# Kernel tuning notes

Measured on AMD Instinct MI355X. Metric: run time of the kernel, lower is better.

## Reference

```python
import jax, jax.numpy as jnp
import numpy as np

N_NODES = 50000
N_EDGES = 800000
IN_FEAT = 96
NUM_CLASSES = 40
K_HOPS = 2        # SGConv K=2
LPA_ITERS = 3     # lpaiters


def setup_inputs() -> dict:
    key = jax.random.key(0)
    ks = jax.random.split(key, 6)
    x = jax.random.normal(ks[0], (N_NODES, IN_FEAT), dtype=jnp.float32)
    edge_index = jax.random.randint(ks[1], (2, N_EDGES), 0, N_NODES, dtype=jnp.int64)
    y = jax.random.randint(ks[2], (N_NODES,), 0, NUM_CLASSES, dtype=jnp.int64)
    mask = jax.random.bernoulli(ks[3], 0.5, (N_NODES,))
    edge_weight = jnp.ones((N_EDGES,), dtype=jnp.float32)  # nn.Parameter(torch.ones(num_edges))
    W = jax.random.normal(ks[4], (IN_FEAT, NUM_CLASSES), dtype=jnp.float32) / np.sqrt(IN_FEAT)
    b = jax.random.normal(ks[5], (NUM_CLASSES,), dtype=jnp.float32) * 0.01
    return {"x": x, "edge_index": edge_index, "y": y, "mask": mask,
            "edge_weight": edge_weight, "W": W, "b": b}


def _gcn_norm_self_loops(edge_index, edge_weight, n):
    # PyG gcn_norm with add_self_loops=True (SGConv default), fill_value=1
    row, col = edge_index[0], edge_index[1]
    loop = jnp.arange(n, dtype=row.dtype)
    row = jnp.concatenate([row, loop])
    col = jnp.concatenate([col, loop])
    w = jnp.concatenate([edge_weight, jnp.ones((n,), edge_weight.dtype)])
    deg = jax.ops.segment_sum(w, col, num_segments=n)
    dinv = jnp.where(deg > 0, deg ** -0.5, 0.0)
    return row, col, dinv[row] * w * dinv[col]


def _propagate(h, row, col, w, n):
    # gather -> weight -> scatter-add (aggr='add' at target nodes)
    return jax.ops.segment_sum(w[:, None] * h[row], col, num_segments=n)


def reference(x, edge_index, y, mask, edge_weight, W, b):
    n = x.shape[0]
    # ---- SGConv(K=2) with learnable edge_weight, gcn_norm with self-loops ----
    row, col, norm = _gcn_norm_self_loops(edge_index, edge_weight, n)
    h = x
    for _ in range(K_HOPS):
        h = _propagate(h, row, col, norm, n)
    x_out = h @ W + b
    # ---- LPAconv: edge_weight given, so NO gcn_norm; raw weighted scatter-add ----
    y1h = jax.nn.one_hot(y, NUM_CLASSES, dtype=jnp.float32)
    out = jnp.where(mask[:, None], y1h, 0.0)  # out[mask] = y[mask]
    r2, c2 = edge_index[0], edge_index[1]
    for _ in range(LPA_ITERS):
        out = _propagate(out, r2, c2, edge_weight, n)
    return (x_out, out)
```

## Files before the change

kernel.cpp:

```cpp
#include <hip/hip_runtime.h>

constexpr int N_NODES     = 50000;
constexpr int N_EDGES     = 800000;
constexpr int IN_FEAT     = 96;
constexpr int NUM_CLASSES = 40;
constexpr int CCH = NUM_CLASSES / 4;
constexpr int CH8 = NUM_CLASSES / 8;
constexpr int SCAN_B = 1024;
constexpr int NSCAN = (N_NODES + SCAN_B - 1) / SCAN_B;

__global__ void rank_k(const int* __restrict__ col, int* __restrict__ cnt,
                       int* __restrict__ rank) {
    int e = blockIdx.x * blockDim.x + threadIdx.x;
    if (e >= N_EDGES) return;
    rank[e] = atomicAdd(&cnt[col[e]], 1);
}

__global__ __launch_bounds__(SCAN_B) void scan1_k(const int* __restrict__ cnt,
                                                  int* __restrict__ pscan,
                                                  int* __restrict__ bsum) {
    __shared__ int buf[SCAN_B];
    int tid = threadIdx.x;
    int i = blockIdx.x * SCAN_B + tid;
    int v = (i < N_NODES) ? cnt[i] : 0;
    buf[tid] = v;
    __syncthreads();
    for (int off = 1; off < SCAN_B; off <<= 1) {
        int t = (tid >= off) ? buf[tid - off] : 0;
        __syncthreads();
        buf[tid] += t;
        __syncthreads();
    }
    if (i < N_NODES) pscan[i] = buf[tid] - v;
    if (tid == SCAN_B - 1) bsum[blockIdx.x] = buf[tid];
}

__global__ void scan2_k(const int* __restrict__ bsum, int* __restrict__ boff,
                        int* __restrict__ rowptr) {
    __shared__ int buf[64];
    int tid = threadIdx.x;
    int v = (tid < NSCAN) ? bsum[tid] : 0;
    buf[tid] = v;
    __syncthreads();
    for (int off = 1; off < 64; off <<= 1) {
        int t = (tid >= off) ? buf[tid - off] : 0;
        __syncthreads();
        buf[tid] += t;
        __syncthreads();
    }
    boff[tid] = buf[tid] - v;
    if (tid == NSCAN - 1) rowptr[N_NODES] = buf[tid];
}

__global__ void scan3_k(const int* __restrict__ pscan, const int* __restrict__ boff,
                        int* __restrict__ rowptr) {
    int i = blockIdx.x * blockDim.x + threadIdx.x;
    if (i < N_NODES) rowptr[i] = boff[i >> 10] + pscan[i];
}

__global__ void fill_k(const int* __restrict__ row, const int* __restrict__ col,
                       const float* __restrict__ ew, const int* __restrict__ rowptr,
                       const int* __restrict__ rank, int2* __restrict__ pair) {
    int e = blockIdx.x * blockDim.x + threadIdx.x;
    if (e >= N_EDGES) return;
    int c = col[e];
    int pos = rowptr[c] + rank[e];
    pair[pos] = make_int2(row[e], __float_as_int(ew[e]));
}

__global__ void node_prep_k(const int* __restrict__ rowptr, const int2* __restrict__ pair,
                            const int* __restrict__ y, const int* __restrict__ mask,
                            float* __restrict__ dinv, int* __restrict__ ym) {
    int i = blockIdx.x * blockDim.x + threadIdx.x;
    if (i >= N_NODES) return;
    int p0 = rowptr[i], p1 = rowptr[i + 1];
    float d = 1.0f;
    for (int p = p0; p < p1; ++p) d += __int_as_float(pair[p].y);
    dinv[i] = d > 0.0f ? rsqrtf(d) : 0.0f;
    ym[i] = (mask[i] != 0) ? y[i] : -1;
}

__global__ __launch_bounds__(256) void xw_k(const float* __restrict__ x,
                                            const float* __restrict__ Wm,
                                            float* __restrict__ xw) {
    __shared__ float4 Ws[IN_FEAT * CCH];
    int tid = threadIdx.x;
    for (int t = tid; t < IN_FEAT * CCH; t += 256)
        Ws[t] = reinterpret_cast<const float4*>(Wm)[t];
    __syncthreads();
    int idx = blockIdx.x * 256 + tid;
    if (idx >= N_NODES * CCH) return;
    int i = idx / CCH;
    int j = idx - i * CCH;
    const float4* xr = reinterpret_cast<const float4*>(x + i * IN_FEAT);
    float4 acc = make_float4(0.f, 0.f, 0.f, 0.f);
#pragma unroll
    for (int f4 = 0; f4 < IN_FEAT / 4; ++f4) {
        float4 xv = xr[f4];
        float4 w0 = Ws[(4 * f4 + 0) * CCH + j];
        float4 w1 = Ws[(4 * f4 + 1) * CCH + j];
        float4 w2 = Ws[(4 * f4 + 2) * CCH + j];
        float4 w3 = Ws[(4 * f4 + 3) * CCH + j];
        acc.x = fmaf(xv.x, w0.x, fmaf(xv.y, w1.x, fmaf(xv.z, w2.x, fmaf(xv.w, w3.x, acc.x))));
        acc.y = fmaf(xv.x, w0.y, fmaf(xv.y, w1.y, fmaf(xv.z, w2.y, fmaf(xv.w, w3.y, acc.y))));
        acc.z = fmaf(xv.x, w0.z, fmaf(xv.y, w1.z, fmaf(xv.z, w2.z, fmaf(xv.w, w3.z, acc.z))));
        acc.w = fmaf(xv.x, w0.w, fmaf(xv.y, w1.w, fmaf(xv.z, w2.w, fmaf(xv.w, w3.w, acc.w))));
    }
    reinterpret_cast<float4*>(xw + i * NUM_CLASSES)[j] = acc;
}

__global__ void fused1_k(const int* __restrict__ rowptr, const int2* __restrict__ pair,
                         const float* __restrict__ dinv, const int* __restrict__ ym,
                         const float* __restrict__ xw,
                         float* __restrict__ g1, float* __restrict__ lA) {
    int idx = blockIdx.x * blockDim.x + threadIdx.x;
    if (idx >= N_NODES * CH8) return;
    int i = idx / CH8;
    int j = idx - i * CH8;
    int p0 = rowptr[i], p1 = rowptr[i + 1];
    float dc = dinv[i];
    float selfw = dc * dc;
    const float4* vr = reinterpret_cast<const float4*>(xw + i * NUM_CLASSES) + 2 * j;
    float4 v0 = vr[0], v1 = vr[1];
    float4 s0 = make_float4(selfw * v0.x, selfw * v0.y, selfw * v0.z, selfw * v0.w);
    float4 s1 = make_float4(selfw * v1.x, selfw * v1.y, selfw * v1.z, selfw * v1.w);
    float4 a0 = make_float4(0.f, 0.f, 0.f, 0.f);
    float4 a1 = make_float4(0.f, 0.f, 0.f, 0.f);
    int base = j << 3;
    for (int p = p0; p < p1; ++p) {
        int2 pr = pair[p];
        int s = pr.x;
        float w = __int_as_float(pr.y);
        float nv = dinv[s] * (w * dc);
        const float4* ur = reinterpret_cast<const float4*>(xw + s * NUM_CLASSES) + 2 * j;
        float4 u0 = ur[0], u1 = ur[1];
        int t = ym[s] - base;
        s0.x = fmaf(nv, u0.x, s0.x); s0.y = fmaf(nv, u0.y, s0.y);
        s0.z = fmaf(nv, u0.z, s0.z); s0.w = fmaf(nv, u0.w, s0.w);
        s1.x = fmaf(nv, u1.x, s1.x); s1.y = fmaf(nv, u1.y, s1.y);
        s1.z = fmaf(nv, u1.z, s1.z); s1.w = fmaf(nv, u1.w, s1.w);
        a0.x += (t == 0) ? w : 0.f; a0.y += (t == 1) ? w : 0.f;
        a0.z += (t == 2) ? w : 0.f; a0.w += (t == 3) ? w : 0.f;
        a1.x += (t == 4) ? w : 0.f; a1.y += (t == 5) ? w : 0.f;
        a1.z += (t == 6) ? w : 0.f; a1.w += (t == 7) ? w : 0.f;
    }
    float4* go = reinterpret_cast<float4*>(g1 + i * NUM_CLASSES) + 2 * j;
    go[0] = s0; go[1] = s1;
    float4* lo = reinterpret_cast<float4*>(lA + i * NUM_CLASSES) + 2 * j;
    lo[0] = a0; lo[1] = a1;
}

__global__ void fused2_k(const int* __restrict__ rowptr, const int2* __restrict__ pair,
                         const float* __restrict__ dinv,
                         const float* __restrict__ g1, const float* __restrict__ lA,
                         const float* __restrict__ bias,
                         float* __restrict__ out, float* __restrict__ lB) {
    int idx = blockIdx.x * blockDim.x + threadIdx.x;
    if (idx >= N_NODES * CH8) return;
    int i = idx / CH8;
    int j = idx - i * CH8;
    int p0 = rowptr[i], p1 = rowptr[i + 1];
    float dc = dinv[i];
    float selfw = dc * dc;
    const float4* vr = reinterpret_cast<const float4*>(g1 + i * NUM_CLASSES) + 2 * j;
    float4 v0 = vr[0], v1 = vr[1];
    float4 s0 = make_float4(selfw * v0.x, selfw * v0.y, selfw * v0.z, selfw * v0.w);
    float4 s1 = make_float4(selfw * v1.x, selfw * v1.y, selfw * v1.z, selfw * v1.w);
    float4 a0 = make_float4(0.f, 0.f, 0.f, 0.f);
    float4 a1 = make_float4(0.f, 0.f, 0.f, 0.f);
    for (int p = p0; p < p1; ++p) {
        int2 pr = pair[p];
        int s = pr.x;
        float w = __int_as_float(pr.y);
        float nv = dinv[s] * (w * dc);
        const float4* ur = reinterpret_cast<const float4*>(g1 + s * NUM_CLASSES) + 2 * j;
        const float4* lr = reinterpret_cast<const float4*>(lA + s * NUM_CLASSES) + 2 * j;
        float4 u0 = ur[0], u1 = ur[1];
        float4 m0 = lr[0], m1 = lr[1];
        s0.x = fmaf(nv, u0.x, s0.x); s0.y = fmaf(nv, u0.y, s0.y);
        s0.z = fmaf(nv, u0.z, s0.z); s0.w = fmaf(nv, u0.w, s0.w);
        s1.x = fmaf(nv, u1.x, s1.x); s1.y = fmaf(nv, u1.y, s1.y);
        s1.z = fmaf(nv, u1.z, s1.z); s1.w = fmaf(nv, u1.w, s1.w);
        a0.x = fmaf(w, m0.x, a0.x); a0.y = fmaf(w, m0.y, a0.y);
        a0.z = fmaf(w, m0.z, a0.z); a0.w = fmaf(w, m0.w, a0.w);
        a1.x = fmaf(w, m1.x, a1.x); a1.y = fmaf(w, m1.y, a1.y);
        a1.z = fmaf(w, m1.z, a1.z); a1.w = fmaf(w, m1.w, a1.w);
    }
    const float4* br = reinterpret_cast<const float4*>(bias) + 2 * j;
    float4 b0 = br[0], b1 = br[1];
    s0.x += b0.x; s0.y += b0.y; s0.z += b0.z; s0.w += b0.w;
    s1.x += b1.x; s1.y += b1.y; s1.z += b1.z; s1.w += b1.w;
    float4* oo = reinterpret_cast<float4*>(out + i * NUM_CLASSES) + 2 * j;
    oo[0] = s0; oo[1] = s1;
    float4* lo = reinterpret_cast<float4*>(lB + i * NUM_CLASSES) + 2 * j;
    lo[0] = a0; lo[1] = a1;
}

__global__ void lpa3_k(const int* __restrict__ rowptr, const int2* __restrict__ pair,
                       const float* __restrict__ lB, float* __restrict__ lout) {
    int idx = blockIdx.x * blockDim.x + threadIdx.x;
    if (idx >= N_NODES * CH8) return;
    int i = idx / CH8;
    int j = idx - i * CH8;
    int p0 = rowptr[i], p1 = rowptr[i + 1];
    float4 a0 = make_float4(0.f, 0.f, 0.f, 0.f);
    float4 a1 = make_float4(0.f, 0.f, 0.f, 0.f);
    for (int p = p0; p < p1; ++p) {
        int2 pr = pair[p];
        int s = pr.x;
        float w = __int_as_float(pr.y);
        const float4* lr = reinterpret_cast<const float4*>(lB + s * NUM_CLASSES) + 2 * j;
        float4 m0 = lr[0], m1 = lr[1];
        a0.x = fmaf(w, m0.x, a0.x); a0.y = fmaf(w, m0.y, a0.y);
        a0.z = fmaf(w, m0.z, a0.z); a0.w = fmaf(w, m0.w, a0.w);
        a1.x = fmaf(w, m1.x, a1.x); a1.y = fmaf(w, m1.y, a1.y);
        a1.z = fmaf(w, m1.z, a1.z); a1.w = fmaf(w, m1.w, a1.w);
    }
    float4* lo = reinterpret_cast<float4*>(lout + i * NUM_CLASSES) + 2 * j;
    lo[0] = a0; lo[1] = a1;
}


extern "C" void kernel_launch(void* const* d_in, const int* in_sizes, int n_in,
                              void* d_out, int out_size, void* d_ws, size_t ws_size,
                              hipStream_t stream) {
    const float* x    = (const float*)d_in[0];
    const int*   ei   = (const int*)d_in[1];
    const int*   row  = ei;
    const int*   col  = ei + N_EDGES;
    const int*   y    = (const int*)d_in[2];
    const int*   mask = (const int*)d_in[3];
    const float* ew   = (const float*)d_in[4];
    const float* Wm   = (const float*)d_in[5];
    const float* bias = (const float*)d_in[6];
    float* out     = (float*)d_out;
    float* lpa_out = out + N_NODES * NUM_CLASSES;

    int*   cnt      = (int*)d_ws;
    int*   pscan    = cnt + 50000;
    int*   bsum     = pscan + 50048;
    int*   boff     = bsum + 64;
    int*   rowptr   = boff + 64;
    int*   rank     = rowptr + 50004;
    int*   ym       = rank + 800000;
    float* dinv     = (float*)(ym + 50000);
    int2*  pair     = (int2*)(dinv + 50000);
    float* xw       = (float*)(pair + 800000);
    float* g1       = xw + (size_t)N_NODES * NUM_CLASSES;
    float* lA       = g1 + (size_t)N_NODES * NUM_CLASSES;
    float* lB       = lA + (size_t)N_NODES * NUM_CLASSES;

    const int B = 256;
    auto g = [](long long n, int b) { return (int)((n + b - 1) / b); };

    hipMemsetAsync(cnt, 0, 50000u * sizeof(int), stream);
    rank_k<<<g(N_EDGES, B), B, 0, stream>>>(col, cnt, rank);
    scan1_k<<<NSCAN, SCAN_B, 0, stream>>>(cnt, pscan, bsum);
    scan2_k<<<1, 64, 0, stream>>>(bsum, boff, rowptr);
    scan3_k<<<g(N_NODES, B), B, 0, stream>>>(pscan, boff, rowptr);
    fill_k<<<g(N_EDGES, B), B, 0, stream>>>(row, col, ew, rowptr, rank, pair);

    node_prep_k<<<g(N_NODES, B), B, 0, stream>>>(rowptr, pair, y, mask, dinv, ym);

    xw_k<<<g((long long)N_NODES * CCH, B), B, 0, stream>>>(x, Wm, xw);

    fused1_k<<<g((long long)N_NODES * CH8, B), B, 0, stream>>>(
        rowptr, pair, dinv, ym, xw, g1, lA);
    fused2_k<<<g((long long)N_NODES * CH8, B), B, 0, stream>>>(
        rowptr, pair, dinv, g1, lA, bias, out, lB);
    lpa3_k<<<g((long long)N_NODES * CH8, B), B, 0, stream>>>(
        rowptr, pair, lB, lpa_out);
}
```

Before: 287.3 us.

## Store intermediate node features in fp16 and vectorize edge preprocessing kernels

Intermediate per-node buffers (xw, g1, lA, lB) are now stored as half precision with rows padded to 64 halves (128 bytes), and converted to float only for the arithmetic. This targets the gather bandwidth of the three propagation kernels, which fetch a 40-wide feature row per edge. The rank and fill kernels also switch to processing four edges per thread with int4 loads. The cost is fp16 rounding in the intermediate values, which could break tolerance, and LPA label counts above the half range could lose precision.

```diff
diff --git a/kernel.cpp b/kernel.cpp
--- a/kernel.cpp
+++ b/kernel.cpp
@@ -1,4 +1,5 @@
 #include <hip/hip_runtime.h>
+#include <hip/hip_fp16.h>
 
 constexpr int N_NODES     = 50000;
 constexpr int N_EDGES     = 800000;
@@ -6,14 +7,38 @@
 constexpr int NUM_CLASSES = 40;
 constexpr int CCH = NUM_CLASSES / 4;
 constexpr int CH8 = NUM_CLASSES / 8;
+constexpr int HS  = 64;
 constexpr int SCAN_B = 1024;
 constexpr int NSCAN = (N_NODES + SCAN_B - 1) / SCAN_B;
 
+__device__ __forceinline__ void h8_to_f(const uint4& u, float4& lo, float4& hi) {
+    float2 f0 = __half22float2(*reinterpret_cast<const __half2*>(&u.x));
+    float2 f1 = __half22float2(*reinterpret_cast<const __half2*>(&u.y));
+    float2 f2 = __half22float2(*reinterpret_cast<const __half2*>(&u.z));
+    float2 f3 = __half22float2(*reinterpret_cast<const __half2*>(&u.w));
+    lo = make_float4(f0.x, f0.y, f1.x, f1.y);
+    hi = make_float4(f2.x, f2.y, f3.x, f3.y);
+}
+__device__ __forceinline__ uint4 f_to_h8(const float4& lo, const float4& hi) {
+    uint4 u;
+    *reinterpret_cast<__half2*>(&u.x) = __floats2half2_rn(lo.x, lo.y);
+    *reinterpret_cast<__half2*>(&u.y) = __floats2half2_rn(lo.z, lo.w);
+    *reinterpret_cast<__half2*>(&u.z) = __floats2half2_rn(hi.x, hi.y);
+    *reinterpret_cast<__half2*>(&u.w) = __floats2half2_rn(hi.z, hi.w);
+    return u;
+}
+
 __global__ void rank_k(const int* __restrict__ col, int* __restrict__ cnt,
                        int* __restrict__ rank) {
-    int e = blockIdx.x * blockDim.x + threadIdx.x;
-    if (e >= N_EDGES) return;
-    rank[e] = atomicAdd(&cnt[col[e]], 1);
+    int t = blockIdx.x * blockDim.x + threadIdx.x;
+    if (t >= N_EDGES / 4) return;
+    int4 c = reinterpret_cast<const int4*>(col)[t];
+    int4 r;
+    r.x = atomicAdd(&cnt[c.x], 1);
+    r.y = atomicAdd(&cnt[c.y], 1);
+    r.z = atomicAdd(&cnt[c.z], 1);
+    r.w = atomicAdd(&cnt[c.w], 1);
+    reinterpret_cast<int4*>(rank)[t] = r;
 }
 
 __global__ __launch_bounds__(SCAN_B) void scan1_k(const int* __restrict__ cnt,
@@ -61,11 +86,16 @@
 __global__ void fill_k(const int* __restrict__ row, const int* __restrict__ col,
                        const float* __restrict__ ew, const int* __restrict__ rowptr,
                        const int* __restrict__ rank, int2* __restrict__ pair) {
-    int e = blockIdx.x * blockDim.x + threadIdx.x;
-    if (e >= N_EDGES) return;
-    int c = col[e];
-    int pos = rowptr[c] + rank[e];
-    pair[pos] = make_int2(row[e], __float_as_int(ew[e]));
+    int t = blockIdx.x * blockDim.x + threadIdx.x;
+    if (t >= N_EDGES / 4) return;
+    int4   c = reinterpret_cast<const int4*>(col)[t];
+    int4   r = reinterpret_cast<const int4*>(row)[t];
+    int4   k = reinterpret_cast<const int4*>(rank)[t];
+    float4 w = reinterpret_cast<const float4*>(ew)[t];
+    pair[rowptr[c.x] + k.x] = make_int2(r.x, __float_as_int(w.x));
+    pair[rowptr[c.y] + k.y] = make_int2(r.y, __float_as_int(w.y));
+    pair[rowptr[c.z] + k.z] = make_int2(r.z, __float_as_int(w.z));
+    pair[rowptr[c.w] + k.w] = make_int2(r.w, __float_as_int(w.w));
 }
 
 __global__ void node_prep_k(const int* __restrict__ rowptr, const int2* __restrict__ pair,
@@ -82,7 +112,7 @@
 
 __global__ __launch_bounds__(256) void xw_k(const float* __restrict__ x,
                                             const float* __restrict__ Wm,
-                                            float* __restrict__ xw) {
+                                            __half* __restrict__ xwh) {
     __shared__ float4 Ws[IN_FEAT * CCH];
     int tid = threadIdx.x;
     for (int t = tid; t < IN_FEAT * CCH; t += 256)
@@ -106,13 +136,16 @@
         acc.z = fmaf(xv.x, w0.z, fmaf(xv.y, w1.z, fmaf(xv.z, w2.z, fmaf(xv.w, w3.z, acc.z))));
         acc.w = fmaf(xv.x, w0.w, fmaf(xv.y, w1.w, fmaf(xv.z, w2.w, fmaf(xv.w, w3.w, acc.w))));
     }
-    reinterpret_cast<float4*>(xw + i * NUM_CLASSES)[j] = acc;
+    uint2 h;
+    *reinterpret_cast<__half2*>(&h.x) = __floats2half2_rn(acc.x, acc.y);
+    *reinterpret_cast<__half2*>(&h.y) = __floats2half2_rn(acc.z, acc.w);
+    reinterpret_cast<uint2*>(xwh + (size_t)i * HS)[j] = h;
 }
 
 __global__ void fused1_k(const int* __restrict__ rowptr, const int2* __restrict__ pair,
                          const float* __restrict__ dinv, const int* __restrict__ ym,
-                         const float* __restrict__ xw,
-                         float* __restrict__ g1, float* __restrict__ lA) {
+                         const __half* __restrict__ xwh,
+                         __half* __restrict__ g1h, __half* __restrict__ lAh) {
     int idx = blockIdx.x * blockDim.x + threadIdx.x;
     if (idx >= N_NODES * CH8) return;
     int i = idx / CH8;
@@ -120,8 +153,8 @@
     int p0 = rowptr[i], p1 = rowptr[i + 1];
     float dc = dinv[i];
     float selfw = dc * dc;
-    const float4* vr = reinterpret_cast<const float4*>(xw + i * NUM_CLASSES) + 2 * j;
-    float4 v0 = vr[0], v1 = vr[1];
+    uint4 vh = *reinterpret_cast<const uint4*>(xwh + (size_t)i * HS + j * 8);
+    float4 v0, v1; h8_to_f(vh, v0, v1);
     float4 s0 = make_float4(selfw * v0.x, selfw * v0.y, selfw * v0.z, selfw * v0.w);
     float4 s1 = make_float4(selfw * v1.x, selfw * v1.y, selfw * v1.z, selfw * v1.w);
     float4 a0 = make_float4(0.f, 0.f, 0.f, 0.f);
@@ -132,8 +165,8 @@
         int s = pr.x;
         float w = __int_as_float(pr.y);
         float nv = dinv[s] * (w * dc);
-        const float4* ur = reinterpret_cast<const float4*>(xw + s * NUM_CLASSES) + 2 * j;
-        float4 u0 = ur[0], u1 = ur[1];
+        uint4 uh = *reinterpret_cast<const uint4*>(xwh + (size_t)s * HS + j * 8);
+        float4 u0, u1; h8_to_f(uh, u0, u1);
         int t = ym[s] - base;
         s0.x = fmaf(nv, u0.x, s0.x); s0.y = fmaf(nv, u0.y, s0.y);
         s0.z = fmaf(nv, u0.z, s0.z); s0.w = fmaf(nv, u0.w, s0.w);
@@ -144,17 +177,15 @@
         a1.x += (t == 4) ? w : 0.f; a1.y += (t == 5) ? w : 0.f;
         a1.z += (t == 6) ? w : 0.f; a1.w += (t == 7) ? w : 0.f;
     }
-    float4* go = reinterpret_cast<float4*>(g1 + i * NUM_CLASSES) + 2 * j;
-    go[0] = s0; go[1] = s1;
-    float4* lo = reinterpret_cast<float4*>(lA + i * NUM_CLASSES) + 2 * j;
-    lo[0] = a0; lo[1] = a1;
+    *reinterpret_cast<uint4*>(g1h + (size_t)i * HS + j * 8) = f_to_h8(s0, s1);
+    *reinterpret_cast<uint4*>(lAh + (size_t)i * HS + j * 8) = f_to_h8(a0, a1);
 }
 
 __global__ void fused2_k(const int* __restrict__ rowptr, const int2* __restrict__ pair,
                          const float* __restrict__ dinv,
-                         const float* __restrict__ g1, const float* __restrict__ lA,
+                         const __half* __restrict__ g1h, const __half* __restrict__ lAh,
                          const float* __restrict__ bias,
-                         float* __restrict__ out, float* __restrict__ lB) {
+                         float* __restrict__ out, __half* __restrict__ lBh) {
     int idx = blockIdx.x * blockDim.x + threadIdx.x;
     if (idx >= N_NODES * CH8) return;
     int i = idx / CH8;
@@ -162,8 +193,8 @@
     int p0 = rowptr[i], p1 = rowptr[i + 1];
     float dc = dinv[i];
     float selfw = dc * dc;
-    const float4* vr = reinterpret_cast<const float4*>(g1 + i * NUM_CLASSES) + 2 * j;
-    float4 v0 = vr[0], v1 = vr[1];
+    uint4 vh = *reinterpret_cast<const uint4*>(g1h + (size_t)i * HS + j * 8);
+    float4 v0, v1; h8_to_f(vh, v0, v1);
     float4 s0 = make_float4(selfw * v0.x, selfw * v0.y, selfw * v0.z, selfw * v0.w);
     float4 s1 = make_float4(selfw * v1.x, selfw * v1.y, selfw * v1.z, selfw * v1.w);
     float4 a0 = make_float4(0.f, 0.f, 0.f, 0.f);
@@ -173,10 +204,10 @@
         int s = pr.x;
         float w = __int_as_float(pr.y);
         float nv = dinv[s] * (w * dc);
-        const float4* ur = reinterpret_cast<const float4*>(g1 + s * NUM_CLASSES) + 2 * j;
-        const float4* lr = reinterpret_cast<const float4*>(lA + s * NUM_CLASSES) + 2 * j;
-        float4 u0 = ur[0], u1 = ur[1];
-        float4 m0 = lr[0], m1 = lr[1];
+        uint4 uh = *reinterpret_cast<const uint4*>(g1h + (size_t)s * HS + j * 8);
+        uint4 mh = *reinterpret_cast<const uint4*>(lAh + (size_t)s * HS + j * 8);
+        float4 u0, u1; h8_to_f(uh, u0, u1);
+        float4 m0, m1; h8_to_f(mh, m0, m1);
         s0.x = fmaf(nv, u0.x, s0.x); s0.y = fmaf(nv, u0.y, s0.y);
         s0.z = fmaf(nv, u0.z, s0.z); s0.w = fmaf(nv, u0.w, s0.w);
         s1.x = fmaf(nv, u1.x, s1.x); s1.y = fmaf(nv, u1.y, s1.y);
@@ -184,20 +215,19 @@
         a0.x = fmaf(w, m0.x, a0.x); a0.y = fmaf(w, m0.y, a0.y);
         a0.z = fmaf(w, m0.z, a0.z); a0.w = fmaf(w, m0.w, a0.w);
         a1.x = fmaf(w, m1.x, a1.x); a1.y = fmaf(w, m1.y, a1.y);
-        a1.z = fmaf(w, m1.z, a1.z); a1.w = fmaf(w, m1.w, a1.w);
+        a1.w = fmaf(w, m1.w, a1.w); a1.z = fmaf(w, m1.z, a1.z);
     }
     const float4* br = reinterpret_cast<const float4*>(bias) + 2 * j;
     float4 b0 = br[0], b1 = br[1];
     s0.x += b0.x; s0.y += b0.y; s0.z += b0.z; s0.w += b0.w;
     s1.x += b1.x; s1.y += b1.y; s1.z += b1.z; s1.w += b1.w;
-    float4* oo = reinterpret_cast<float4*>(out + i * NUM_CLASSES) + 2 * j;
+    float4* oo = reinterpret_cast<float4*>(out + (size_t)i * NUM_CLASSES) + 2 * j;
     oo[0] = s0; oo[1] = s1;
-    float4* lo = reinterpret_cast<float4*>(lB + i * NUM_CLASSES) + 2 * j;
-    lo[0] = a0; lo[1] = a1;
+    *reinterpret_cast<uint4*>(lBh + (size_t)i * HS + j * 8) = f_to_h8(a0, a1);
 }
 
 __global__ void lpa3_k(const int* __restrict__ rowptr, const int2* __restrict__ pair,
-                       const float* __restrict__ lB, float* __restrict__ lout) {
+                       const __half* __restrict__ lBh, float* __restrict__ lout) {
     int idx = blockIdx.x * blockDim.x + threadIdx.x;
     if (idx >= N_NODES * CH8) return;
     int i = idx / CH8;
@@ -209,14 +239,14 @@
         int2 pr = pair[p];
         int s = pr.x;
         float w = __int_as_float(pr.y);
-        const float4* lr = reinterpret_cast<const float4*>(lB + s * NUM_CLASSES) + 2 * j;
-        float4 m0 = lr[0], m1 = lr[1];
+        uint4 mh = *reinterpret_cast<const uint4*>(lBh + (size_t)s * HS + j * 8);
+        float4 m0, m1; h8_to_f(mh, m0, m1);
         a0.x = fmaf(w, m0.x, a0.x); a0.y = fmaf(w, m0.y, a0.y);
         a0.z = fmaf(w, m0.z, a0.z); a0.w = fmaf(w, m0.w, a0.w);
         a1.x = fmaf(w, m1.x, a1.x); a1.y = fmaf(w, m1.y, a1.y);
         a1.z = fmaf(w, m1.z, a1.z); a1.w = fmaf(w, m1.w, a1.w);
     }
-    float4* lo = reinterpret_cast<float4*>(lout + i * NUM_CLASSES) + 2 * j;
+    float4* lo = reinterpret_cast<float4*>(lout + (size_t)i * NUM_CLASSES) + 2 * j;
     lo[0] = a0; lo[1] = a1;
 }
 
@@ -236,38 +266,38 @@
     float* out     = (float*)d_out;
     float* lpa_out = out + N_NODES * NUM_CLASSES;
 
-    int*   cnt      = (int*)d_ws;
-    int*   pscan    = cnt + 50000;
-    int*   bsum     = pscan + 50048;
-    int*   boff     = bsum + 64;
-    int*   rowptr   = boff + 64;
-    int*   rank     = rowptr + 50004;
-    int*   ym       = rank + 800000;
-    float* dinv     = (float*)(ym + 50000);
-    int2*  pair     = (int2*)(dinv + 50000);
-    float* xw       = (float*)(pair + 800000);
-    float* g1       = xw + (size_t)N_NODES * NUM_CLASSES;
-    float* lA       = g1 + (size_t)N_NODES * NUM_CLASSES;
-    float* lB       = lA + (size_t)N_NODES * NUM_CLASSES;
+    int*    cnt    = (int*)d_ws;
+    int*    pscan  = cnt + 50000;
+    int*    bsum   = pscan + 50048;
+    int*    boff   = bsum + 64;
+    int*    rowptr = boff + 64;
+    int*    rank   = rowptr + 50004;
+    int*    ym     = rank + 800000;
+    float*  dinv   = (float*)(ym + 50000);
+    int2*   pair   = (int2*)(dinv + 50000);
+    __half* xwh    = (__half*)(pair + 800000);
+    __half* g1h    = xwh + (size_t)N_NODES * HS;
+    __half* lAh    = g1h + (size_t)N_NODES * HS;
+    __half* lBh    = lAh + (size_t)N_NODES * HS;
 
     const int B = 256;
     auto g = [](long long n, int b) { return (int)((n + b - 1) / b); };
 
     hipMemsetAsync(cnt, 0, 50000u * sizeof(int), stream);
-    rank_k<<<g(N_EDGES, B), B, 0, stream>>>(col, cnt, rank);
+    rank_k<<<g(N_EDGES / 4, B), B, 0, stream>>>(col, cnt, rank);
     scan1_k<<<NSCAN, SCAN_B, 0, stream>>>(cnt, pscan, bsum);
     scan2_k<<<1, 64, 0, stream>>>(bsum, boff, rowptr);
     scan3_k<<<g(N_NODES, B), B, 0, stream>>>(pscan, boff, rowptr);
-    fill_k<<<g(N_EDGES, B), B, 0, stream>>>(row, col, ew, rowptr, rank, pair);
+    fill_k<<<g(N_EDGES / 4, B), B, 0, stream>>>(row, col, ew, rowptr, rank, pair);
 
     node_prep_k<<<g(N_NODES, B), B, 0, stream>>>(rowptr, pair, y, mask, dinv, ym);
 
-    xw_k<<<g((long long)N_NODES * CCH, B), B, 0, stream>>>(x, Wm, xw);
+    xw_k<<<g((long long)N_NODES * CCH, B), B, 0, stream>>>(x, Wm, xwh);
 
     fused1_k<<<g((long long)N_NODES * CH8, B), B, 0, stream>>>(
-        rowptr, pair, dinv, ym, xw, g1, lA);
+        rowptr, pair, dinv, ym, xwh, g1h, lAh);
     fused2_k<<<g((long long)N_NODES * CH8, B), B, 0, stream>>>(
-        rowptr, pair, dinv, g1, lA, bias, out, lB);
+        rowptr, pair, dinv, g1h, lAh, bias, out, lBh);
     lpa3_k<<<g((long long)N_NODES * CH8, B), B, 0, stream>>>(
-        rowptr, pair, lB, lpa_out);
-}
+        rowptr, pair, lBh, lpa_out);
+}
```

After: 245.2 us. 1.17x faster.
